# Optimization experiments

Hardware: AMD Instinct MI355X
Metric: run time of the kernel (lower is better)

The kernel has to match this reference:

```python
import jax, jax.numpy as jnp
import numpy as np

B, I, O, D, H = 64, 1152, 32, 8, 16
NUM_ITERS = 3


def squash(s, axis=-1, eps=1e-08):
    sq = jnp.sum(s * s, axis=axis, keepdims=True)
    return (sq / (1.0 + sq)) * s / jnp.sqrt(sq + eps)


def setup_inputs() -> dict:
    key = jax.random.key(0)
    k1, k2 = jax.random.split(key)
    u = jax.random.normal(k1, (B, I, D), dtype=jnp.float32)
    weight = jax.random.normal(k2, (I, O, D, H), dtype=jnp.float32) * 0.1
    return {"u": u, "weight": weight}


def reference(u, weight):
    # u_hat: [b, i, o, h]
    u_hat = jnp.einsum('bid,iodh->bioh', u, weight)
    logits = jnp.zeros(u_hat.shape[:3], dtype=u_hat.dtype)

    def body(logits, _):
        coupling = jax.nn.softmax(logits, axis=-1)        # [b,i,o]
        s = jnp.einsum('bio,bioh->boh', coupling, u_hat)  # [b,o,h]
        v = squash(s)                                     # [b,o,h]
        logits = logits + jnp.einsum('boh,bioh->bio', v, u_hat)
        return logits, v

    _, vs = jax.lax.scan(body, logits, None, length=NUM_ITERS)
    return vs[-1]
```

## Files before the change

kernel.cpp:

```cpp
#include <hip/hip_runtime.h>

#define BB 64
#define II 1152
#define OO 32
#define DD 8
#define HH 16
#define BOH (BB * OO * HH)
#define WTILE (OO * DD * HH)

#define IC   9
#define NIC  128
#define NBB  16
#define NBG  4
#define NJB  4

#define NBBF 4
#define NBGF 16

typedef _Float16 half8 __attribute__((ext_vector_type(8)));

#define UHN ((size_t)BB * II * OO * HH)

template<int CTRL>
__device__ __forceinline__ float dpp_add(float x)
{
    return x + __int_as_float(__builtin_amdgcn_update_dpp(
            0, __float_as_int(x), CTRL, 0xF, 0xF, false));
}

__device__ __forceinline__ float row_sum16(float x)
{
    x = dpp_add<0x121>(x);
    x = dpp_add<0x122>(x);
    x = dpp_add<0x124>(x);
    x = dpp_add<0x128>(x);
    return x;
}

__device__ __forceinline__ float add_xor32(float x)
{
#if __has_builtin(__builtin_amdgcn_permlane32_swap)
    auto r = __builtin_amdgcn_permlane32_swap(
        __float_as_uint(x), __float_as_uint(x), false, false);
    return __uint_as_float(r[0]) + __uint_as_float(r[1]);
#else
    return x + __shfl_xor(x, 32, 64);
#endif
}

__device__ __forceinline__ float add_xor16(float x)
{
#if __has_builtin(__builtin_amdgcn_permlane16_swap)
    auto r = __builtin_amdgcn_permlane16_swap(
        __float_as_uint(x), __float_as_uint(x), false, false);
    return __uint_as_float(r[0]) + __uint_as_float(r[1]);
#else
    return x + __int_as_float(__builtin_amdgcn_ds_swizzle(__float_as_int(x), 0x401F));
#endif
}

__device__ __forceinline__ int wswz(int f) { return f ^ (((f >> 7) & 31) << 2); }

__device__ __forceinline__ void stage_w_tile(const float* __restrict__ wg,
                                             float* __restrict__ wn, int tid)
{
    #pragma unroll
    for (int j = 0; j < 4; j++) {
        const int P = (tid + j * 256) * 4;
        const int g = wswz(P);
        __builtin_amdgcn_global_load_lds(
            (const __attribute__((address_space(1))) void*)(wg + g),
            (__attribute__((address_space(3))) void*)(wn + P),
            16, 0, 0);
    }
}

template<int PASS, bool ATOMIC, bool UHAT>
__global__ __launch_bounds__(256)
void pass_kernel(const float* __restrict__ u, const float* __restrict__ w,
                 const float* __restrict__ pv0, const float* __restrict__ pv1,
                 float* __restrict__ out, _Float16* __restrict__ uhat)
{
    __shared__ __align__(16) float Wsh[2][WTILE];

    const int tid   = threadIdx.x;
    const int o     = tid & 31;
    const int hh    = (tid >> 5) & 1;
    const int bq    = tid >> 6;
    const int bbase = blockIdx.y * NBB;
    const int i0    = blockIdx.x * IC;
    const int hofs  = hh * 8;
    const int swm   = o << 2;
    const int orow  = o * (DD * HH);

    stage_w_tile(w + (size_t)i0 * WTILE, Wsh[0], tid);

    float vsum[NJB][8];
    if (PASS >= 1) {
        #pragma unroll
        for (int jb = 0; jb < NJB; jb++) {
            const int b = bbase + bq * NJB + jb;
            const float* p = pv0 + ((b * OO + o) * HH + hofs);
            float4 a = *(const float4*)p;
            float4 c = *(const float4*)(p + 4);
            vsum[jb][0] = a.x; vsum[jb][1] = a.y; vsum[jb][2] = a.z; vsum[jb][3] = a.w;
            vsum[jb][4] = c.x; vsum[jb][5] = c.y; vsum[jb][6] = c.z; vsum[jb][7] = c.w;
            if (PASS == 2) {
                const float* q = pv1 + ((b * OO + o) * HH + hofs);
                float4 a2 = *(const float4*)q;
                float4 c2 = *(const float4*)(q + 4);
                vsum[jb][0] += a2.x; vsum[jb][1] += a2.y; vsum[jb][2] += a2.z; vsum[jb][3] += a2.w;
                vsum[jb][4] += c2.x; vsum[jb][5] += c2.y; vsum[jb][6] += c2.z; vsum[jb][7] += c2.w;
            }
        }
    }

    float sacc[NJB][8];
    #pragma unroll
    for (int jb = 0; jb < NJB; jb++)
        #pragma unroll
        for (int h2 = 0; h2 < 8; h2++) sacc[jb][h2] = 0.f;

    __syncthreads();

    for (int ii = 0; ii < IC; ii++) {
        const float* wcur = Wsh[ii & 1];

        if (ii + 1 < IC)
            stage_w_tile(w + (size_t)(i0 + ii + 1) * WTILE, Wsh[(ii + 1) & 1], tid);

        float us[NJB][8];
        #pragma unroll
        for (int jb = 0; jb < NJB; jb++) {
            const float* ub = u + ((size_t)(bbase + bq * NJB + jb) * II + (i0 + ii)) * DD;
            float4 a = *(const float4*)ub;
            float4 c = *(const float4*)(ub + 4);
            us[jb][0] = a.x; us[jb][1] = a.y; us[jb][2] = a.z; us[jb][3] = a.w;
            us[jb][4] = c.x; us[jb][5] = c.y; us[jb][6] = c.z; us[jb][7] = c.w;
        }

        float uh[NJB][8];
        #pragma unroll
        for (int jb = 0; jb < NJB; jb++)
            #pragma unroll
            for (int h2 = 0; h2 < 8; h2++) uh[jb][h2] = 0.f;
        #pragma unroll
        for (int d = 0; d < DD; d++) {
            const int ba  = (d * HH + hofs    ) ^ swm;
            const int bb2 = (d * HH + hofs + 4) ^ swm;
            float4 wa = *(const float4*)&wcur[orow + ba];
            float4 wb = *(const float4*)&wcur[orow + bb2];
            const float wv[8] = {wa.x, wa.y, wa.z, wa.w, wb.x, wb.y, wb.z, wb.w};
            #pragma unroll
            for (int jb = 0; jb < NJB; jb++)
                #pragma unroll
                for (int h2 = 0; h2 < 8; h2++)
                    uh[jb][h2] = fmaf(us[jb][d], wv[h2], uh[jb][h2]);
        }

        if (UHAT) {
            #pragma unroll
            for (int jb = 0; jb < NJB; jb++) {
                const int b = bbase + bq * NJB + jb;
                half8 hv;
                #pragma unroll
                for (int h2 = 0; h2 < 8; h2++) hv[h2] = (_Float16)uh[jb][h2];
                *(half8*)(uhat + (((size_t)b * II + (i0 + ii)) * OO + o) * HH + hofs) = hv;
            }
        }

        float cc[NJB];
        if (PASS == 0) {
            #pragma unroll
            for (int jb = 0; jb < NJB; jb++) cc[jb] = 1.0f / 32.0f;
        } else {
            #pragma unroll
            for (int jb = 0; jb < NJB; jb++) {
                float lg = 0.f;
                #pragma unroll
                for (int h2 = 0; h2 < 8; h2++)
                    lg = fmaf(vsum[jb][h2], uh[jb][h2], lg);
                lg = add_xor32(lg);
                const float e = __expf(lg);
                const float se = add_xor16(row_sum16(e));
                cc[jb] = __fdividef(e, se);
            }
        }

        #pragma unroll
        for (int jb = 0; jb < NJB; jb++)
            #pragma unroll
            for (int h2 = 0; h2 < 8; h2++)
                sacc[jb][h2] = fmaf(cc[jb], uh[jb][h2], sacc[jb][h2]);

        __syncthreads();
    }

    #pragma unroll
    for (int jb = 0; jb < NJB; jb++) {
        const int b = bbase + bq * NJB + jb;
        if (ATOMIC) {
            float* p = out + ((b * OO + o) * HH + hofs);
            #pragma unroll
            for (int h2 = 0; h2 < 8; h2++) atomicAdd(p + h2, sacc[jb][h2]);
        } else {
            float* p = out + ((size_t)blockIdx.x * BB + b) * (OO * HH) + o * HH + hofs;
            *(float4*)p       = make_float4(sacc[jb][0], sacc[jb][1], sacc[jb][2], sacc[jb][3]);
            *(float4*)(p + 4) = make_float4(sacc[jb][4], sacc[jb][5], sacc[jb][6], sacc[jb][7]);
        }
    }
}

template<int PASS>
__global__ __launch_bounds__(256)
void fast_pass_kernel(const _Float16* __restrict__ uhat,
                      const float* __restrict__ pv0, const float* __restrict__ pv1,
                      float* __restrict__ out)
{
    const int tid  = threadIdx.x;
    const int o    = tid & 31;
    const int hh   = (tid >> 5) & 1;
    const int bq   = tid >> 6;
    const int b    = blockIdx.y * NBBF + bq;
    const int i0   = blockIdx.x * IC;
    const int hofs = hh * 8;

    half8 hv[IC];
    #pragma unroll
    for (int ii = 0; ii < IC; ii++)
        hv[ii] = *(const half8*)
            (uhat + (((size_t)b * II + (i0 + ii)) * OO + o) * HH + hofs);

    float vsum[8];
    {
        const float* p = pv0 + ((b * OO + o) * HH + hofs);
        float4 a = *(const float4*)p;
        float4 c = *(const float4*)(p + 4);
        vsum[0] = a.x; vsum[1] = a.y; vsum[2] = a.z; vsum[3] = a.w;
        vsum[4] = c.x; vsum[5] = c.y; vsum[6] = c.z; vsum[7] = c.w;
        if (PASS == 2) {
            const float* q = pv1 + ((b * OO + o) * HH + hofs);
            float4 a2 = *(const float4*)q;
            float4 c2 = *(const float4*)(q + 4);
            vsum[0] += a2.x; vsum[1] += a2.y; vsum[2] += a2.z; vsum[3] += a2.w;
            vsum[4] += c2.x; vsum[5] += c2.y; vsum[6] += c2.z; vsum[7] += c2.w;
        }
    }

    float sacc[8];
    #pragma unroll
    for (int h2 = 0; h2 < 8; h2++) sacc[h2] = 0.f;

    #pragma unroll
    for (int ii = 0; ii < IC; ii++) {
        float uh[8];
        #pragma unroll
        for (int h2 = 0; h2 < 8; h2++) uh[h2] = (float)hv[ii][h2];

        float lg = 0.f;
        #pragma unroll
        for (int h2 = 0; h2 < 8; h2++)
            lg = fmaf(vsum[h2], uh[h2], lg);
        lg = add_xor32(lg);
        const float e = __expf(lg);
        const float se = add_xor16(row_sum16(e));
        const float cc = __fdividef(e, se);

        #pragma unroll
        for (int h2 = 0; h2 < 8; h2++)
            sacc[h2] = fmaf(cc, uh[h2], sacc[h2]);
    }

    float* p = out + ((size_t)blockIdx.x * BB + b) * (OO * HH) + o * HH + hofs;
    *(float4*)p       = make_float4(sacc[0], sacc[1], sacc[2], sacc[3]);
    *(float4*)(p + 4) = make_float4(sacc[4], sacc[5], sacc[6], sacc[7]);
}

__global__ __launch_bounds__(256)
void reduce_squash_wide_kernel(const float* __restrict__ part, float* __restrict__ v)
{
    const int t4l = threadIdx.x & 31;
    const int icp = threadIdx.x >> 5;
    const int t4  = blockIdx.x * 32 + t4l;

    const float4* p = (const float4*)part + t4;
    float4 acc = make_float4(0.f, 0.f, 0.f, 0.f);
    #pragma unroll
    for (int k = 0; k < NIC / 8; k++) {
        float4 x = p[(size_t)(icp * (NIC / 8) + k) * (BOH / 4)];
        acc.x += x.x; acc.y += x.y; acc.z += x.z; acc.w += x.w;
    }

    __shared__ float4 red[8][32];
    red[icp][t4l] = acc;
    __syncthreads();

    if (threadIdx.x < 32) {
        float4 a = red[0][t4l];
        #pragma unroll
        for (int j = 1; j < 8; j++) {
            float4 x = red[j][t4l];
            a.x += x.x; a.y += x.y; a.z += x.z; a.w += x.w;
        }
        float sq = a.x * a.x + a.y * a.y + a.z * a.z + a.w * a.w;
        sq = dpp_add<0xB1>(sq);
        sq = dpp_add<0x4E>(sq);
        const float scale = (sq / (1.f + sq)) * rsqrtf(sq + 1e-8f);
        a.x *= scale; a.y *= scale; a.z *= scale; a.w *= scale;
        ((float4*)v)[t4] = a;
    }
}

__global__ __launch_bounds__(256)
void squash_kernel(const float* __restrict__ s, float* __restrict__ v)
{
    const int t = blockIdx.x * blockDim.x + threadIdx.x;
    if (t >= BB * OO) return;
    const float4* sp = (const float4*)(s + t * HH);
    float4 a = sp[0], b = sp[1], c = sp[2], d = sp[3];
    float sq = a.x*a.x + a.y*a.y + a.z*a.z + a.w*a.w
             + b.x*b.x + b.y*b.y + b.z*b.z + b.w*b.w
             + c.x*c.x + c.y*c.y + c.z*c.z + c.w*c.w
             + d.x*d.x + d.y*d.y + d.z*d.z + d.w*d.w;
    const float scale = (sq / (1.f + sq)) * rsqrtf(sq + 1e-8f);
    a.x *= scale; a.y *= scale; a.z *= scale; a.w *= scale;
    b.x *= scale; b.y *= scale; b.z *= scale; b.w *= scale;
    c.x *= scale; c.y *= scale; c.z *= scale; c.w *= scale;
    d.x *= scale; d.y *= scale; d.z *= scale; d.w *= scale;
    float4* vp = (float4*)(v + t * HH);
    vp[0] = a; vp[1] = b; vp[2] = c; vp[3] = d;
}

extern "C" void kernel_launch(void* const* d_in, const int* in_sizes, int n_in,
                              void* d_out, int out_size, void* d_ws, size_t ws_size,
                              hipStream_t stream)
{
    (void)in_sizes; (void)n_in; (void)out_size;
    const float* u = (const float*)d_in[0];
    const float* w = (const float*)d_in[1];
    float* out = (float*)d_out;

    const size_t partN = (size_t)NIC * BOH;
    const size_t need  = (partN + 2 * BOH) * sizeof(float) + UHN * sizeof(_Float16);
    const dim3 blk(256);

    if (ws_size >= need) {
        float* part     = (float*)d_ws;
        float* v0       = part + partN;
        float* v1       = v0 + BOH;
        _Float16* uhat  = (_Float16*)(v1 + BOH);
        const int rblocks = BOH / 4 / 32;

        pass_kernel<0, false, true><<<dim3(NIC, NBG), blk, 0, stream>>>(
            u, w, nullptr, nullptr, part, uhat);
        reduce_squash_wide_kernel<<<rblocks, 256, 0, stream>>>(part, v0);
        fast_pass_kernel<1><<<dim3(NIC, NBGF), blk, 0, stream>>>(uhat, v0, nullptr, part);
        reduce_squash_wide_kernel<<<rblocks, 256, 0, stream>>>(part, v1);
        fast_pass_kernel<2><<<dim3(NIC, NBGF), blk, 0, stream>>>(uhat, v0, v1, part);
        reduce_squash_wide_kernel<<<rblocks, 256, 0, stream>>>(part, out);
    } else {
        float* s0 = (float*)d_ws;
        float* s1 = s0 + BOH;
        float* v0 = s1 + BOH;
        float* v1 = v0 + BOH;
        hipMemsetAsync(d_ws, 0, 2 * BOH * sizeof(float), stream);
        hipMemsetAsync(d_out, 0, BOH * sizeof(float), stream);
        const dim3 grid(NIC, NBG);
        const int sq_blocks = (BB * OO + 255) / 256;

        pass_kernel<0, true, false><<<grid, blk, 0, stream>>>(u, w, nullptr, nullptr, s0, nullptr);
        squash_kernel<<<sq_blocks, 256, 0, stream>>>(s0, v0);
        pass_kernel<1, true, false><<<grid, blk, 0, stream>>>(u, w, v0, nullptr, s1, nullptr);
        squash_kernel<<<sq_blocks, 256, 0, stream>>>(s1, v1);
        pass_kernel<2, true, false><<<grid, blk, 0, stream>>>(u, w, v0, v1, out, nullptr);
        squash_kernel<<<sq_blocks, 256, 0, stream>>>(out, out);
    }
}
```

Baseline: 127.2 us.

## Reduce routing passes in-block over i ranges to shrink partial-sum traffic

Each block of the routing passes now handles one batch element and 36 consecutive input capsules, split over four 64-thread groups. The groups' partial sums are combined in shared memory before one write. This leaves 32 partial slices instead of 128, so partial-buffer writes and the reads in the following reduce-squash kernel drop by about four times. The cost is a block barrier and shared-memory reduction per block, and each block now covers a single batch element.

New measurement: 120.7 us, median of 2. -5.1%, faster.

```diff
diff --git a/kernel.cpp b/kernel.cpp
--- a/kernel.cpp
+++ b/kernel.cpp
@@ -14,8 +14,8 @@
 #define NBG  4
 #define NJB  4
 
-#define NBBF 4
-#define NBGF 16
+#define NRNG 32
+#define ICR  (II / NRNG)
 
 typedef _Float16 half8 __attribute__((ext_vector_type(8)));
 
@@ -215,19 +215,21 @@
 __global__ __launch_bounds__(256)
 void fast_pass_kernel(const _Float16* __restrict__ uhat,
                       const float* __restrict__ pv0, const float* __restrict__ pv1,
-                      float* __restrict__ out)
-{
+                      float* __restrict__ part)
+{
+    __shared__ float4 red[4][64][2];
+
     const int tid  = threadIdx.x;
     const int o    = tid & 31;
     const int hh   = (tid >> 5) & 1;
-    const int bq   = tid >> 6;
-    const int b    = blockIdx.y * NBBF + bq;
-    const int i0   = blockIdx.x * IC;
+    const int q    = tid >> 6;
+    const int b    = blockIdx.y;
+    const int i0   = blockIdx.x * ICR + q * 9;
     const int hofs = hh * 8;
 
-    half8 hv[IC];
-    #pragma unroll
-    for (int ii = 0; ii < IC; ii++)
+    half8 hv[9];
+    #pragma unroll
+    for (int ii = 0; ii < 9; ii++)
         hv[ii] = *(const half8*)
             (uhat + (((size_t)b * II + (i0 + ii)) * OO + o) * HH + hofs);
 
@@ -239,9 +241,9 @@
         vsum[0] = a.x; vsum[1] = a.y; vsum[2] = a.z; vsum[3] = a.w;
         vsum[4] = c.x; vsum[5] = c.y; vsum[6] = c.z; vsum[7] = c.w;
         if (PASS == 2) {
-            const float* q = pv1 + ((b * OO + o) * HH + hofs);
-            float4 a2 = *(const float4*)q;
-            float4 c2 = *(const float4*)(q + 4);
+            const float* qq = pv1 + ((b * OO + o) * HH + hofs);
+            float4 a2 = *(const float4*)qq;
+            float4 c2 = *(const float4*)(qq + 4);
             vsum[0] += a2.x; vsum[1] += a2.y; vsum[2] += a2.z; vsum[3] += a2.w;
             vsum[4] += c2.x; vsum[5] += c2.y; vsum[6] += c2.z; vsum[7] += c2.w;
         }
@@ -252,7 +254,7 @@
     for (int h2 = 0; h2 < 8; h2++) sacc[h2] = 0.f;
 
     #pragma unroll
-    for (int ii = 0; ii < IC; ii++) {
+    for (int ii = 0; ii < 9; ii++) {
         float uh[8];
         #pragma unroll
         for (int h2 = 0; h2 < 8; h2++) uh[h2] = (float)hv[ii][h2];
@@ -271,11 +273,26 @@
             sacc[h2] = fmaf(cc, uh[h2], sacc[h2]);
     }
 
-    float* p = out + ((size_t)blockIdx.x * BB + b) * (OO * HH) + o * HH + hofs;
-    *(float4*)p       = make_float4(sacc[0], sacc[1], sacc[2], sacc[3]);
-    *(float4*)(p + 4) = make_float4(sacc[4], sacc[5], sacc[6], sacc[7]);
-}
-
+    red[q][o + 32 * hh][0] = make_float4(sacc[0], sacc[1], sacc[2], sacc[3]);
+    red[q][o + 32 * hh][1] = make_float4(sacc[4], sacc[5], sacc[6], sacc[7]);
+    __syncthreads();
+
+    if (tid < 64) {
+        float4 a = red[0][tid][0], c = red[0][tid][1];
+        #pragma unroll
+        for (int j = 1; j < 4; j++) {
+            float4 x = red[j][tid][0], y = red[j][tid][1];
+            a.x += x.x; a.y += x.y; a.z += x.z; a.w += x.w;
+            c.x += y.x; c.y += y.y; c.z += y.z; c.w += y.w;
+        }
+        float* p = part + ((size_t)blockIdx.x * BB + b) * (OO * HH)
+                 + (tid & 31) * HH + (tid >> 5) * 8;
+        *(float4*)p       = a;
+        *(float4*)(p + 4) = c;
+    }
+}
+
+template<int NCH>
 __global__ __launch_bounds__(256)
 void reduce_squash_wide_kernel(const float* __restrict__ part, float* __restrict__ v)
 {
@@ -286,8 +303,8 @@
     const float4* p = (const float4*)part + t4;
     float4 acc = make_float4(0.f, 0.f, 0.f, 0.f);
     #pragma unroll
-    for (int k = 0; k < NIC / 8; k++) {
-        float4 x = p[(size_t)(icp * (NIC / 8) + k) * (BOH / 4)];
+    for (int k = 0; k < NCH / 8; k++) {
+        float4 x = p[(size_t)(icp * (NCH / 8) + k) * (BOH / 4)];
         acc.x += x.x; acc.y += x.y; acc.z += x.z; acc.w += x.w;
     }
 
@@ -353,11 +370,11 @@
 
         pass_kernel<0, false, true><<<dim3(NIC, NBG), blk, 0, stream>>>(
             u, w, nullptr, nullptr, part, uhat);
-        reduce_squash_wide_kernel<<<rblocks, 256, 0, stream>>>(part, v0);
-        fast_pass_kernel<1><<<dim3(NIC, NBGF), blk, 0, stream>>>(uhat, v0, nullptr, part);
-        reduce_squash_wide_kernel<<<rblocks, 256, 0, stream>>>(part, v1);
-        fast_pass_kernel<2><<<dim3(NIC, NBGF), blk, 0, stream>>>(uhat, v0, v1, part);
-        reduce_squash_wide_kernel<<<rblocks, 256, 0, stream>>>(part, out);
+        reduce_squash_wide_kernel<NIC><<<rblocks, 256, 0, stream>>>(part, v0);
+        fast_pass_kernel<1><<<dim3(NRNG, BB), blk, 0, stream>>>(uhat, v0, nullptr, part);
+        reduce_squash_wide_kernel<NRNG><<<rblocks, 256, 0, stream>>>(part, v1);
+        fast_pass_kernel<2><<<dim3(NRNG, BB), blk, 0, stream>>>(uhat, v0, v1, part);
+        reduce_squash_wide_kernel<NRNG><<<rblocks, 256, 0, stream>>>(part, out);
     } else {
         float* s0 = (float*)d_ws;
         float* s1 = s0 + BOH;
```
